# Kernel optimization log

Measured on AMD Instinct MI355X. Metric: run time of the kernel, lower is better.

The kernel has to match this reference:

```python
import jax, jax.numpy as jnp
import numpy as np

N, E, D, R = 50000, 600000, 128, 8


def setup_inputs() -> dict:
    key = jax.random.key(0)
    ks = jax.random.split(key, 10)
    return {
        "x": jax.random.normal(ks[0], (N, D), dtype=jnp.float32),
        "h": jax.random.normal(ks[1], (N, D), dtype=jnp.float32),
        "edge_index": jax.random.randint(ks[2], (2, E), 0, N, dtype=jnp.int32),
        "edge_type": jax.random.randint(ks[3], (E,), 0, R, dtype=jnp.int32),
        "edge_weight": jax.random.uniform(ks[4], (E,), dtype=jnp.float32),
        "rel_weight": jax.random.normal(ks[5], (R, D, D), dtype=jnp.float32) * 0.05,
        "root_weight": jax.random.normal(ks[6], (D, D), dtype=jnp.float32) * 0.05,
        "bias": jax.random.normal(ks[7], (D,), dtype=jnp.float32) * 0.05,
        "skip_weight": jax.random.normal(ks[8], (D, D), dtype=jnp.float32) * 0.05,
        "skip_bias": jax.random.normal(ks[9], (D,), dtype=jnp.float32) * 0.05,
    }


def reference(x, h, edge_index, edge_type, edge_weight, rel_weight, root_weight, bias, skip_weight, skip_bias):
    # skip projection (nn.Linear: y = x W^T + b)
    skip = x @ skip_weight.T + skip_bias  # [N, D]

    src, dst = edge_index[0], edge_index[1]  # PyG: message from src (x_j), aggregated at dst

    # Transform every node by every relation once (R is small), then gather per edge.
    # Avoids per-edge [E, D, D] weight gather.
    h_rel = jnp.einsum('nd,rdf->nrf', h, rel_weight)  # [N, R, D]
    msg = h_rel[src, edge_type] * edge_weight[:, None]  # [E, D]

    agg = jax.ops.segment_sum(msg, dst, num_segments=h.shape[0])  # [N, D]

    out = agg + h @ root_weight + bias + skip
    return out
```

## Files before the change

kernel.cpp:

```cpp
#include <hip/hip_runtime.h>


constexpr int DIM  = 128;
constexpr int BM   = 64;
constexpr int KC   = 32;
constexpr int BPAD = 4;
constexpr int KTOT = 1280;
constexpr int SCAN_CHUNK = 2048;

typedef __attribute__((ext_vector_type(8))) short     short8v;
typedef __attribute__((ext_vector_type(8))) unsigned short ushort8v;
typedef __attribute__((ext_vector_type(4))) float     float4v;
typedef __attribute__((ext_vector_type(4))) unsigned  uint4v;

__device__ __forceinline__ unsigned short f2bf(float x) {
    union { float f; unsigned u; } c; c.f = x;
    unsigned u = c.u;
    u += 0x7fffu + ((u >> 16) & 1u);
    return (unsigned short)(u >> 16);
}
__device__ __forceinline__ float bits2f(unsigned u) {
    union { unsigned u; float f; } c; c.u = u; return c.f;
}

__device__ __forceinline__ void gload_lds16(const void* g, void* l) {
    __builtin_amdgcn_global_load_lds(
        (const __attribute__((address_space(1))) unsigned int*)g,
        (__attribute__((address_space(3))) unsigned int*)l,
        16, 0, 0);
}

__global__ __launch_bounds__(256) void prep_kernel(
    const float* __restrict__ h, const float* __restrict__ x,
    const float* __restrict__ relF, const float* __restrict__ rootW,
    const float* __restrict__ skipW,
    unsigned short* __restrict__ hb, unsigned short* __restrict__ xb,
    unsigned short* __restrict__ Bt, int n8, int nb1)
{
    const int b = blockIdx.x;
    if (b < 2 * nb1) {
        const float* __restrict__ src = (b < nb1) ? h : x;
        unsigned short* __restrict__ dst = (b < nb1) ? hb : xb;
        int i = (b < nb1 ? b : b - nb1) * 256 + threadIdx.x;
        if (i >= n8) return;
        const float4 v0 = *reinterpret_cast<const float4*>(src + (size_t)i * 8);
        const float4 v1 = *reinterpret_cast<const float4*>(src + (size_t)i * 8 + 4);
        ushort8v o;
        o[0] = f2bf(v0.x); o[1] = f2bf(v0.y); o[2] = f2bf(v0.z); o[3] = f2bf(v0.w);
        o[4] = f2bf(v1.x); o[5] = f2bf(v1.y); o[6] = f2bf(v1.z); o[7] = f2bf(v1.w);
        *reinterpret_cast<ushort8v*>(dst + (size_t)i * 8) = o;
    } else {
        int idx = (b - 2 * nb1) * 256 + threadIdx.x;
        if (idx >= DIM * KTOT) return;
        int f = idx / KTOT, k = idx % KTOT;
        float v;
        if (k < 1024)       v = relF[(size_t)k * DIM + f];
        else if (k < 1152)  v = rootW[(k - 1024) * DIM + f];
        else                v = skipW[f * DIM + (k - 1152)];
        Bt[(size_t)f * KTOT + k] = f2bf(v);
    }
}

__global__ __launch_bounds__(256) void zero_i32_kernel(int* __restrict__ p, int n)
{
    int i = blockIdx.x * 256 + threadIdx.x;
    if (i < n) p[i] = 0;
}

__global__ __launch_bounds__(256) void hist_kernel(
    const int* __restrict__ ei, const int* __restrict__ et,
    int* __restrict__ counts, int E)
{
    int e = blockIdx.x * 256 + threadIdx.x;
    if (e < E) atomicAdd(&counts[ei[(long long)E + e] * 8 + (et[e] & 7)], 1);
}

__global__ __launch_bounds__(256) void scan1_kernel(
    const int* __restrict__ counts, int* __restrict__ local,
    int* __restrict__ blockSums, int M)
{
    __shared__ int sh[256];
    const int b = blockIdx.x, t = threadIdx.x;
    const int base = b * SCAN_CHUNK + t * 8;

    int v[8];
    int s = 0;
    #pragma unroll
    for (int j = 0; j < 8; ++j) {
        int idx = base + j;
        v[j] = (idx < M) ? counts[idx] : 0;
        s += v[j];
    }
    sh[t] = s;
    __syncthreads();
    for (int off = 1; off < 256; off <<= 1) {
        int x = (t >= off) ? sh[t - off] : 0;
        __syncthreads();
        sh[t] += x;
        __syncthreads();
    }
    int ex = sh[t] - s;
    if (t == 255) blockSums[b] = sh[255];
    #pragma unroll
    for (int j = 0; j < 8; ++j) {
        int idx = base + j;
        if (idx < M) { local[idx] = ex; ex += v[j]; }
    }
}

__global__ __launch_bounds__(1024) void scan2_kernel(int* __restrict__ bs, int nb)
{
    __shared__ int sh[1024];
    const int t = threadIdx.x;
    int v = (t < nb) ? bs[t] : 0;
    sh[t] = v;
    __syncthreads();
    for (int off = 1; off < 1024; off <<= 1) {
        int x = (t >= off) ? sh[t - off] : 0;
        __syncthreads();
        sh[t] += x;
        __syncthreads();
    }
    if (t < nb) bs[t] = sh[t] - v;
}

__global__ __launch_bounds__(256) void scan3_kernel(
    int* __restrict__ offsets, const int* __restrict__ blockSums,
    int* __restrict__ cursor, int M, int E)
{
    const int b = blockIdx.x, t = threadIdx.x;
    const int add = blockSums[b];
    #pragma unroll
    for (int j = 0; j < 8; ++j) {
        int idx = b * SCAN_CHUNK + j * 256 + t;
        if (idx < M) {
            int v = offsets[idx] + add;
            offsets[idx] = v;
            cursor[idx]  = v;
        }
    }
    if (b == 0 && t == 0) offsets[M] = E;
}

__global__ __launch_bounds__(256) void scatter_kernel(
    const int* __restrict__ ei, const int* __restrict__ et,
    const float* __restrict__ ew, int* __restrict__ cursor,
    int2* __restrict__ payload, int E)
{
    int e = blockIdx.x * 256 + threadIdx.x;
    if (e < E) {
        int key = ei[(long long)E + e] * 8 + (et[e] & 7);
        int pos = atomicAdd(&cursor[key], 1);
        payload[pos] = make_int2(ei[e], __float_as_int(ew[e]));
    }
}

__global__ __launch_bounds__(256) void accum_kernel(
    const int2* __restrict__ payload, const unsigned short* __restrict__ hb,
    const int* __restrict__ offsets, unsigned short* __restrict__ S, int M)
{
    const int tid = threadIdx.x;
    const int q   = blockIdx.x * 16 + (tid >> 4);
    const int l16 = tid & 15;
    if (q >= M) return;

    const int s0 = offsets[q];
    const int s1 = offsets[q + 1];

    float acc[8] = {0.f, 0.f, 0.f, 0.f, 0.f, 0.f, 0.f, 0.f};
    int o = s0;
    for (; o + 2 <= s1; o += 2) {
        const int2 p0 = payload[o];
        const int2 p1 = payload[o + 1];
        const uint4v h0 = *reinterpret_cast<const uint4v*>(
            hb + (size_t)p0.x * DIM + l16 * 8);
        const uint4v h1 = *reinterpret_cast<const uint4v*>(
            hb + (size_t)p1.x * DIM + l16 * 8);
        const float w0 = __int_as_float(p0.y);
        const float w1 = __int_as_float(p1.y);
        #pragma unroll
        for (int i = 0; i < 4; ++i) {
            acc[2 * i]     += w0 * bits2f(h0[i] << 16)
                            + w1 * bits2f(h1[i] << 16);
            acc[2 * i + 1] += w0 * bits2f(h0[i] & 0xffff0000u)
                            + w1 * bits2f(h1[i] & 0xffff0000u);
        }
    }
    if (o < s1) {
        const int2 p0 = payload[o];
        const uint4v h0 = *reinterpret_cast<const uint4v*>(
            hb + (size_t)p0.x * DIM + l16 * 8);
        const float w0 = __int_as_float(p0.y);
        #pragma unroll
        for (int i = 0; i < 4; ++i) {
            acc[2 * i]     += w0 * bits2f(h0[i] << 16);
            acc[2 * i + 1] += w0 * bits2f(h0[i] & 0xffff0000u);
        }
    }

    uint4v pk;
    #pragma unroll
    for (int i = 0; i < 4; ++i)
        pk[i] = (unsigned)f2bf(acc[2 * i]) | ((unsigned)f2bf(acc[2 * i + 1]) << 16);
    *reinterpret_cast<uint4v*>(&S[(size_t)q * 128 + l16 * 8]) = pk;
}

__global__ __launch_bounds__(256) void mfma_gemm_kernel(
    const unsigned short* __restrict__ S, const unsigned short* __restrict__ hb,
    const unsigned short* __restrict__ xb, const unsigned short* __restrict__ Bt,
    const float* __restrict__ bias, const float* __restrict__ skipB,
    float* __restrict__ out, int N)
{
    __shared__ unsigned short As[64 * 64];
    __shared__ unsigned short Bs[128 * 64];

    const int tid  = threadIdx.x;
    const int lane = tid & 63;
    const int wid  = tid >> 6;
    const int wr   = wid >> 1, wc = wid & 1;
    const int l15  = lane & 15, l4 = lane >> 4;
    const int n0   = blockIdx.x * 64;

    int aRow[2], aC8[2];
    #pragma unroll
    for (int i = 0; i < 2; ++i) {
        int c = wid * 128 + i * 64 + lane;
        aRow[i] = c >> 3;
        aC8[i]  = (c & 7) ^ (aRow[i] & 7);
    }
    int aN[2];
    #pragma unroll
    for (int i = 0; i < 2; ++i) {
        int n = n0 + aRow[i];
        aN[i] = (n < N) ? n : (N - 1);
    }
    int bCol[4], bC8[4];
    #pragma unroll
    for (int i = 0; i < 4; ++i) {
        int c = wid * 256 + i * 64 + lane;
        bCol[i] = c >> 3;
        bC8[i]  = (c & 7) ^ (bCol[i] & 7);
    }

    float4v acc[2][4];
    #pragma unroll
    for (int m = 0; m < 2; ++m)
        #pragma unroll
        for (int nn = 0; nn < 4; ++nn)
            acc[m][nn] = (float4v)0.f;

    for (int t = 0; t < 20; ++t) {
        const int k0 = t * 64;
        const unsigned short* __restrict__ A;
        size_t strideA;
        int kb;
        if (t < 16)      { A = S;  strideA = 1024; kb = k0; }
        else if (t < 18) { A = hb; strideA = DIM;  kb = k0 - 1024; }
        else             { A = xb; strideA = DIM;  kb = k0 - 1152; }

        __syncthreads();
        #pragma unroll
        for (int i = 0; i < 2; ++i) {
            gload_lds16(A + (size_t)aN[i] * strideA + kb + aC8[i] * 8,
                        (char*)As + (size_t)(wid * 128 + i * 64) * 16);
        }
        #pragma unroll
        for (int i = 0; i < 4; ++i) {
            gload_lds16(Bt + (size_t)bCol[i] * KTOT + k0 + bC8[i] * 8,
                        (char*)Bs + (size_t)(wid * 256 + i * 64) * 16);
        }
        __syncthreads();

        #pragma unroll
        for (int s = 0; s < 2; ++s) {
            const int kk = s * 32 + l4 * 8;
            short8v a[2], b[4];
            #pragma unroll
            for (int m = 0; m < 2; ++m) {
                int row = wr * 32 + m * 16 + l15;
                int bo = row * 128 + ((kk * 2) ^ ((row & 7) << 4));
                a[m] = *reinterpret_cast<const short8v*>((const char*)As + bo);
            }
            #pragma unroll
            for (int nn = 0; nn < 4; ++nn) {
                int col = wc * 64 + nn * 16 + l15;
                int bo = col * 128 + ((kk * 2) ^ ((col & 7) << 4));
                b[nn] = *reinterpret_cast<const short8v*>((const char*)Bs + bo);
            }
            #pragma unroll
            for (int m = 0; m < 2; ++m)
                #pragma unroll
                for (int nn = 0; nn < 4; ++nn)
                    acc[m][nn] = __builtin_amdgcn_mfma_f32_16x16x32_bf16(
                        a[m], b[nn], acc[m][nn], 0, 0, 0);
        }
    }

    #pragma unroll
    for (int nn = 0; nn < 4; ++nn) {
        const int col = wc * 64 + nn * 16 + l15;
        const float bb = bias[col] + skipB[col];
        #pragma unroll
        for (int m = 0; m < 2; ++m) {
            #pragma unroll
            for (int j = 0; j < 4; ++j) {
                int row = wr * 32 + m * 16 + l4 * 4 + j;
                int n = n0 + row;
                if (n < N)
                    out[(size_t)n * DIM + col] = acc[m][nn][j] + bb;
            }
        }
    }
}

__global__ __launch_bounds__(256) void base_kernel(
    const float* __restrict__ x, const float* __restrict__ h,
    const float* __restrict__ skipW, const float* __restrict__ rootW,
    const float* __restrict__ bias, const float* __restrict__ skipB,
    float* __restrict__ out, int N)
{
    __shared__ float As2[BM][KC];
    __shared__ float Bs2[KC][DIM + BPAD];

    const int tid = threadIdx.x;
    const int n0  = blockIdx.x * BM;
    const int f0  = (tid & 31) * 4;
    const int r0  = (tid >> 5) * 8;

    float acc[8][4] = {};

    for (int phase = 0; phase < 2; ++phase) {
        const float* __restrict__ A = phase ? h : x;
        for (int d0 = 0; d0 < DIM; d0 += KC) {
            __syncthreads();
            for (int idx = tid; idx < BM * KC; idx += 256) {
                int r = idx / KC, dd = idx % KC;
                int n = n0 + r;
                As2[r][dd] = (n < N) ? A[(long long)n * DIM + d0 + dd] : 0.f;
            }
            if (phase == 0) {
                for (int idx = tid; idx < DIM * KC; idx += 256) {
                    int f = idx / KC, dd = idx % KC;
                    Bs2[dd][f] = skipW[f * DIM + d0 + dd];
                }
            } else {
                for (int idx = tid; idx < KC * DIM; idx += 256) {
                    int dd = idx / DIM, f = idx % DIM;
                    Bs2[dd][f] = rootW[(d0 + dd) * DIM + f];
                }
            }
            __syncthreads();
            #pragma unroll
            for (int dd = 0; dd < KC; ++dd) {
                float a[8];
                #pragma unroll
                for (int i = 0; i < 8; ++i) a[i] = As2[r0 + i][dd];
                const float4 b = *reinterpret_cast<const float4*>(&Bs2[dd][f0]);
                #pragma unroll
                for (int i = 0; i < 8; ++i) {
                    acc[i][0] += a[i] * b.x; acc[i][1] += a[i] * b.y;
                    acc[i][2] += a[i] * b.z; acc[i][3] += a[i] * b.w;
                }
            }
        }
    }

    float bb[4];
    #pragma unroll
    for (int j = 0; j < 4; ++j) bb[j] = bias[f0 + j] + skipB[f0 + j];
    #pragma unroll
    for (int i = 0; i < 8; ++i) {
        int n = n0 + r0 + i;
        if (n < N) {
            float4 v = make_float4(acc[i][0] + bb[0], acc[i][1] + bb[1],
                                   acc[i][2] + bb[2], acc[i][3] + bb[3]);
            *reinterpret_cast<float4*>(&out[(long long)n * DIM + f0]) = v;
        }
    }
}

__global__ __launch_bounds__(256) void hrel_kernel(
    const float* __restrict__ h, const float* __restrict__ rel,
    float* __restrict__ hrel, int N, int R)
{
    __shared__ float As2[BM][KC];
    __shared__ float Bs2[KC][DIM + BPAD];

    const int tid = threadIdx.x;
    const int n0  = blockIdx.x * BM;
    const int rr  = blockIdx.y;
    const float* __restrict__ B = rel + (size_t)rr * DIM * DIM;
    const int f0  = (tid & 31) * 4;
    const int r0  = (tid >> 5) * 8;

    float acc[8][4] = {};

    for (int d0 = 0; d0 < DIM; d0 += KC) {
        __syncthreads();
        for (int idx = tid; idx < BM * KC; idx += 256) {
            int r = idx / KC, dd = idx % KC;
            int n = n0 + r;
            As2[r][dd] = (n < N) ? h[(long long)n * DIM + d0 + dd] : 0.f;
        }
        for (int idx = tid; idx < KC * DIM; idx += 256) {
            int dd = idx / DIM, f = idx % DIM;
            Bs2[dd][f] = B[(d0 + dd) * DIM + f];
        }
        __syncthreads();
        #pragma unroll
        for (int dd = 0; dd < KC; ++dd) {
            float a[8];
            #pragma unroll
            for (int i = 0; i < 8; ++i) a[i] = As2[r0 + i][dd];
            const float4 b = *reinterpret_cast<const float4*>(&Bs2[dd][f0]);
            #pragma unroll
            for (int i = 0; i < 8; ++i) {
                acc[i][0] += a[i] * b.x; acc[i][1] += a[i] * b.y;
                acc[i][2] += a[i] * b.z; acc[i][3] += a[i] * b.w;
            }
        }
    }

    #pragma unroll
    for (int i = 0; i < 8; ++i) {
        int n = n0 + r0 + i;
        if (n < N) {
            float4 v = make_float4(acc[i][0], acc[i][1], acc[i][2], acc[i][3]);
            *reinterpret_cast<float4*>(&hrel[((long long)n * R + rr) * DIM + f0]) = v;
        }
    }
}

__global__ __launch_bounds__(256) void edge_kernel(
    const int* __restrict__ ei, const int* __restrict__ et,
    const float* __restrict__ ew, const float* __restrict__ hrel,
    float* __restrict__ out, int E, int R)
{
    const int tid  = threadIdx.x;
    const int lane = tid & 31;
    const long long e = (long long)blockIdx.x * 8 + (tid >> 5);
    if (e >= E) return;

    const int   src = ei[e];
    const int   dst = ei[(long long)E + e];
    const int   r   = et[e];
    const float w   = ew[e];

    const float4 v = reinterpret_cast<const float4*>(
        hrel + ((long long)src * R + r) * DIM)[lane];

    float* o = out + (long long)dst * DIM + lane * 4;
    atomicAdd(o + 0, v.x * w);
    atomicAdd(o + 1, v.y * w);
    atomicAdd(o + 2, v.z * w);
    atomicAdd(o + 3, v.w * w);
}

__global__ __launch_bounds__(256) void edge_direct_kernel(
    const int* __restrict__ ei, const int* __restrict__ et,
    const float* __restrict__ ew, const float* __restrict__ h,
    const float* __restrict__ rel, float* __restrict__ out, int E)
{
    const int wid  = threadIdx.x >> 6;
    const int lane = threadIdx.x & 63;
    const long long e = (long long)blockIdx.x * 4 + wid;
    if (e >= E) return;

    const int   src = ei[e];
    const int   dst = ei[(long long)E + e];
    const int   r   = et[e];
    const float w   = ew[e];

    const float* __restrict__ hrow = h + (long long)src * DIM;
    const float* __restrict__ W    = rel + (size_t)r * DIM * DIM;

    float acc0 = 0.f, acc1 = 0.f;
    #pragma unroll 8
    for (int d = 0; d < DIM; ++d) {
        float hv = hrow[d];
        acc0 += hv * W[d * DIM + lane];
        acc1 += hv * W[d * DIM + lane + 64];
    }
    atomicAdd(&out[(long long)dst * DIM + lane],      acc0 * w);
    atomicAdd(&out[(long long)dst * DIM + lane + 64], acc1 * w);
}

extern "C" void kernel_launch(void* const* d_in, const int* in_sizes, int n_in,
                              void* d_out, int out_size, void* d_ws, size_t ws_size,
                              hipStream_t stream)
{
    const float* x     = (const float*)d_in[0];
    const float* h     = (const float*)d_in[1];
    const int*   ei    = (const int*)  d_in[2];
    const int*   et    = (const int*)  d_in[3];
    const float* ew    = (const float*)d_in[4];
    const float* rel   = (const float*)d_in[5];
    const float* rootW = (const float*)d_in[6];
    const float* bias  = (const float*)d_in[7];
    const float* skipW = (const float*)d_in[8];
    const float* skipB = (const float*)d_in[9];
    float* out = (float*)d_out;

    const int N = in_sizes[0] / DIM;
    const int E = in_sizes[3];
    const int R = in_sizes[5] / (DIM * DIM);

    const int M = N * 8;
    const int nbScan = (M + SCAN_CHUNK - 1) / SCAN_CHUNK;

    const size_t S_elems  = (size_t)N * 1024;
    const size_t hb_elems = (size_t)N * DIM;
    const size_t Bt_elems = (size_t)DIM * KTOT;
    const size_t head_bytes =
        (S_elems + 2 * hb_elems + Bt_elems) * sizeof(unsigned short);
    const size_t need_new = head_bytes
                          + (size_t)E * sizeof(int2)
                          + ((size_t)(M + 1) + M + 1024) * sizeof(int);

    if (R == 8 && nbScan <= 1024 && (head_bytes % 8 == 0) && ws_size >= need_new) {
        unsigned short* S  = (unsigned short*)d_ws;
        unsigned short* hb = S + S_elems;
        unsigned short* xb = hb + hb_elems;
        unsigned short* Bt = xb + hb_elems;
        int2*  payload   = (int2*)((char*)d_ws + head_bytes);
        int*   offsets   = (int*)(payload + E);
        int*   cursor    = offsets + (M + 1);
        int*   blockSums = cursor + M;

        const int n8  = N * DIM / 8;
        const int nb1 = (n8 + 255) / 256;
        const int nbB = (DIM * KTOT + 255) / 256;

        zero_i32_kernel<<<dim3((M + 255) / 256), 256, 0, stream>>>(cursor, M);
        hist_kernel<<<dim3((E + 255) / 256), 256, 0, stream>>>(ei, et, cursor, E);
        scan1_kernel<<<dim3(nbScan), 256, 0, stream>>>(cursor, offsets, blockSums, M);
        scan2_kernel<<<dim3(1), 1024, 0, stream>>>(blockSums, nbScan);
        scan3_kernel<<<dim3(nbScan), 256, 0, stream>>>(offsets, blockSums, cursor, M, E);
        scatter_kernel<<<dim3((E + 255) / 256), 256, 0, stream>>>(
            ei, et, ew, cursor, payload, E);
        prep_kernel<<<dim3(2 * nb1 + nbB), 256, 0, stream>>>(
            h, x, rel, rootW, skipW, hb, xb, Bt, n8, nb1);
        accum_kernel<<<dim3((M + 15) / 16), 256, 0, stream>>>(
            payload, hb, offsets, S, M);
        mfma_gemm_kernel<<<dim3((N + 63) / 64), 256, 0, stream>>>(
            S, hb, xb, Bt, bias, skipB, out, N);
    } else {
        base_kernel<<<dim3((N + BM - 1) / BM), 256, 0, stream>>>(
            x, h, skipW, rootW, bias, skipB, out, N);
        if (ws_size >= (size_t)N * R * DIM * sizeof(float)) {
            float* hrel = (float*)d_ws;
            hrel_kernel<<<dim3((N + BM - 1) / BM, R), 256, 0, stream>>>(h, rel, hrel, N, R);
            edge_kernel<<<dim3((E + 7) / 8), 256, 0, stream>>>(ei, et, ew, hrel, out, E, R);
        } else {
            edge_direct_kernel<<<dim3((E + 3) / 4), 256, 0, stream>>>(ei, et, ew, h, rel, out, E);
        }
    }
}
```

Baseline: 162.7 us.

## Shrink GEMM tile to 32 rows with two waves, use memset for cursor zeroing

The MFMA GEMM is retiled from 64 rows and 4 waves to 32 rows and 2 waves per block. Each wave now covers all 32 rows and a 64-column slice, so the grid doubles to about 1563 blocks and fills the CUs better. The trade-off is that every block reloads the full B tile for only half as many rows, which roughly doubles B traffic through global memory and LDS per output. The custom zero kernel is also replaced by hipMemsetAsync.

```diff
diff --git a/kernel.cpp b/kernel.cpp
--- a/kernel.cpp
+++ b/kernel.cpp
@@ -61,12 +61,6 @@
     }
 }
 
-__global__ __launch_bounds__(256) void zero_i32_kernel(int* __restrict__ p, int n)
-{
-    int i = blockIdx.x * 256 + threadIdx.x;
-    if (i < n) p[i] = 0;
-}
-
 __global__ __launch_bounds__(256) void hist_kernel(
     const int* __restrict__ ei, const int* __restrict__ et,
     int* __restrict__ counts, int E)
@@ -205,39 +199,34 @@
     *reinterpret_cast<uint4v*>(&S[(size_t)q * 128 + l16 * 8]) = pk;
 }
 
-__global__ __launch_bounds__(256) void mfma_gemm_kernel(
+__global__ __launch_bounds__(128) void mfma_gemm_kernel(
     const unsigned short* __restrict__ S, const unsigned short* __restrict__ hb,
     const unsigned short* __restrict__ xb, const unsigned short* __restrict__ Bt,
     const float* __restrict__ bias, const float* __restrict__ skipB,
     float* __restrict__ out, int N)
 {
-    __shared__ unsigned short As[64 * 64];
+    __shared__ unsigned short As[32 * 64];
     __shared__ unsigned short Bs[128 * 64];
 
     const int tid  = threadIdx.x;
     const int lane = tid & 63;
     const int wid  = tid >> 6;
-    const int wr   = wid >> 1, wc = wid & 1;
     const int l15  = lane & 15, l4 = lane >> 4;
-    const int n0   = blockIdx.x * 64;
-
-    int aRow[2], aC8[2];
+    const int n0   = blockIdx.x * 32;
+
+    int aC8[2], aN[2];
     #pragma unroll
     for (int i = 0; i < 2; ++i) {
-        int c = wid * 128 + i * 64 + lane;
-        aRow[i] = c >> 3;
-        aC8[i]  = (c & 7) ^ (aRow[i] & 7);
-    }
-    int aN[2];
-    #pragma unroll
-    for (int i = 0; i < 2; ++i) {
-        int n = n0 + aRow[i];
-        aN[i] = (n < N) ? n : (N - 1);
-    }
-    int bCol[4], bC8[4];
-    #pragma unroll
-    for (int i = 0; i < 4; ++i) {
-        int c = wid * 256 + i * 64 + lane;
+        int c   = i * 128 + tid;
+        int row = c >> 3;
+        aC8[i]  = (c & 7) ^ (row & 7);
+        int n   = n0 + row;
+        aN[i]   = (n < N) ? n : (N - 1);
+    }
+    int bCol[8], bC8[8];
+    #pragma unroll
+    for (int i = 0; i < 8; ++i) {
+        int c   = i * 128 + tid;
         bCol[i] = c >> 3;
         bC8[i]  = (c & 7) ^ (bCol[i] & 7);
     }
@@ -262,12 +251,12 @@
         #pragma unroll
         for (int i = 0; i < 2; ++i) {
             gload_lds16(A + (size_t)aN[i] * strideA + kb + aC8[i] * 8,
-                        (char*)As + (size_t)(wid * 128 + i * 64) * 16);
-        }
-        #pragma unroll
-        for (int i = 0; i < 4; ++i) {
+                        (char*)As + (size_t)(i * 128 + wid * 64) * 16);
+        }
+        #pragma unroll
+        for (int i = 0; i < 8; ++i) {
             gload_lds16(Bt + (size_t)bCol[i] * KTOT + k0 + bC8[i] * 8,
-                        (char*)Bs + (size_t)(wid * 256 + i * 64) * 16);
+                        (char*)Bs + (size_t)(i * 128 + wid * 64) * 16);
         }
         __syncthreads();
 
@@ -277,13 +266,13 @@
             short8v a[2], b[4];
             #pragma unroll
             for (int m = 0; m < 2; ++m) {
-                int row = wr * 32 + m * 16 + l15;
+                int row = m * 16 + l15;
                 int bo = row * 128 + ((kk * 2) ^ ((row & 7) << 4));
                 a[m] = *reinterpret_cast<const short8v*>((const char*)As + bo);
             }
             #pragma unroll
             for (int nn = 0; nn < 4; ++nn) {
-                int col = wc * 64 + nn * 16 + l15;
+                int col = wid * 64 + nn * 16 + l15;
                 int bo = col * 128 + ((kk * 2) ^ ((col & 7) << 4));
                 b[nn] = *reinterpret_cast<const short8v*>((const char*)Bs + bo);
             }
@@ -298,13 +287,13 @@
 
     #pragma unroll
     for (int nn = 0; nn < 4; ++nn) {
-        const int col = wc * 64 + nn * 16 + l15;
+        const int col = wid * 64 + nn * 16 + l15;
         const float bb = bias[col] + skipB[col];
         #pragma unroll
         for (int m = 0; m < 2; ++m) {
             #pragma unroll
             for (int j = 0; j < 4; ++j) {
-                int row = wr * 32 + m * 16 + l4 * 4 + j;
+                int row = m * 16 + l4 * 4 + j;
                 int n = n0 + row;
                 if (n < N)
                     out[(size_t)n * DIM + col] = acc[m][nn][j] + bb;
@@ -531,7 +520,7 @@
         const int nb1 = (n8 + 255) / 256;
         const int nbB = (DIM * KTOT + 255) / 256;
 
-        zero_i32_kernel<<<dim3((M + 255) / 256), 256, 0, stream>>>(cursor, M);
+        hipMemsetAsync(cursor, 0, (size_t)M * sizeof(int), stream);
         hist_kernel<<<dim3((E + 255) / 256), 256, 0, stream>>>(ei, et, cursor, E);
         scan1_kernel<<<dim3(nbScan), 256, 0, stream>>>(cursor, offsets, blockSums, M);
         scan2_kernel<<<dim3(1), 1024, 0, stream>>>(blockSums, nbScan);
@@ -542,7 +531,7 @@
             h, x, rel, rootW, skipW, hb, xb, Bt, n8, nb1);
         accum_kernel<<<dim3((M + 15) / 16), 256, 0, stream>>>(
             payload, hb, offsets, S, M);
-        mfma_gemm_kernel<<<dim3((N + 63) / 64), 256, 0, stream>>>(
+        mfma_gemm_kernel<<<dim3((N + 31) / 32), 128, 0, stream>>>(
             S, hb, xb, Bt, bias, skipB, out, N);
     } else {
         base_kernel<<<dim3((N + BM - 1) / BM), 256, 0, stream>>>(
```

New measurement: 173.3 us. 6.5% more time.
